# Kernel optimization log

Measured on AMD Instinct MI355X. Metric: run time of the kernel, lower is better.

## Reference

```python
import jax, jax.numpy as jnp
import numpy as np
import math

B, K, M, D = 8192, 16, 16, 256
LAMBDA_FGW = 0.5
TAU_KL = 0.1
N_OUTER = 5
N_SINKHORN = 10


def setup_inputs() -> dict:
    key = jax.random.key(0)
    ks = jax.random.split(key, 8)
    return {
        'slots_q': jax.random.normal(ks[0], (B, K, D), jnp.float32),
        'slots_r': jax.random.normal(ks[1], (B, M, D), jnp.float32),
        'mask_q': jnp.ones((B, K), jnp.float32),
        'mask_r': jnp.ones((B, M), jnp.float32),
        'centroids_q': jax.random.uniform(ks[2], (B, K, 2), jnp.float32),
        'centroids_r': jax.random.uniform(ks[3], (B, M, 2), jnp.float32),
        'W1': jax.random.normal(ks[4], (D, D), jnp.float32) * 0.05,
        'b1': jnp.zeros((D,), jnp.float32),
        'W2': jax.random.normal(ks[5], (D, D), jnp.float32) * 0.05,
        'b2': jnp.zeros((D,), jnp.float32),
        'log_eps': jnp.asarray(math.log(0.05), jnp.float32),
    }


def _pdist(a, b):
    # ||a_i - b_j||, clamped like torch: clamp(sumsq, 1e-6).sqrt()
    d2 = (jnp.sum(a * a, -1)[:, :, None] + jnp.sum(b * b, -1)[:, None, :]
          - 2.0 * jnp.einsum('bkd,bmd->bkm', a, b))
    return jnp.sqrt(jnp.clip(d2, 1e-6, None))


def reference(slots_q, slots_r, mask_q, mask_r, centroids_q, centroids_r,
              W1, b1, W2, b2, log_eps):
    proj = lambda x: jax.nn.relu(x @ W1.T + b1) @ W2.T + b2
    pq, pr = proj(slots_q), proj(slots_r)
    C = _pdist(pq, pr)                      # [B,K,M]
    Sq = _pdist(centroids_q, centroids_q)   # [B,K,K]
    Sr = _pdist(centroids_r, centroids_r)   # [B,M,M]

    mu = mask_q / (jnp.sum(mask_q, -1, keepdims=True) + 1e-8)
    nu = mask_r / (jnp.sum(mask_r, -1, keepdims=True) + 1e-8)
    T = mu[:, :, None] * nu[:, None, :]

    eps = jnp.clip(jnp.exp(log_eps), 0.01, 0.5)
    rho = TAU_KL / (TAU_KL + eps)
    log_mu = jnp.log(jnp.clip(mu, 1e-8, None))
    log_nu = jnpp = jnp.log(jnp.clip(nu, 1e-8, None))
    Sq2, Sr2 = Sq * Sq, Sr * Sr

    C_fgw = C
    for _ in range(N_OUTER):
        t1 = jnp.einsum('bkl,bl->bk', Sq2, T.sum(2))[:, :, None]
        t2 = jnp.einsum('bm,bmn->bn', T.sum(1), Sr2)[:, None, :]
        t3 = -2.0 * jnp.einsum('bkl,blm,bmn->bkn', Sq, T, Sr)
        L_gw = t1 + t2 + t3
        C_fgw = (1.0 - LAMBDA_FGW) * C + LAMBDA_FGW * L_gw
        log_K = -C_fgw / eps
        log_u = jnp.zeros_like(mu)
        log_v = jnp.zeros_like(nu)
        for _ in range(N_SINKHORN):
            log_u = rho * (log_mu - jax.nn.logsumexp(log_K + log_v[:, None, :], axis=2))
            log_v = rho * (log_nu - jax.nn.logsumexp(log_K + log_u[:, :, None], axis=1))
        T = jnp.exp(log_u[:, :, None] + log_K + log_v[:, None, :])

    cost = jnp.sum(T * C_fgw, axis=(-1, -2))
    return (jax.nn.sigmoid(-cost), T, C, cost)
```

## Files before the change

### kernel.cpp

```cpp
#include <hip/hip_runtime.h>


#define OFF_T   8192
#define OFF_C   2105344
#define OFF_CST 4202496

typedef float  f32x4  __attribute__((ext_vector_type(4)));
typedef float  f32x16 __attribute__((ext_vector_type(16)));
typedef short  s16x8  __attribute__((ext_vector_type(8)));

#define LOG2E 1.4426950408889634f

__device__ __forceinline__ float fexp2(float x) { return __builtin_amdgcn_exp2f(x); }
__device__ __forceinline__ float flog2(float x) { return __builtin_amdgcn_logf(x); }

__device__ __forceinline__ unsigned int cvt_pk_bf16(float lo, float hi) {
  unsigned int r;
  asm("v_cvt_pk_bf16_f32 %0, %1, %2" : "=v"(r) : "v"(lo), "v"(hi));
  return r;
}
__device__ __forceinline__ unsigned short cvt_bf16(float x) {
  unsigned int r;
  asm("v_cvt_pk_bf16_f32 %0, %1, %2" : "=v"(r) : "v"(x), "v"(x));
  return (unsigned short)r;
}

template <int CTRL>
__device__ __forceinline__ float dpp_add(float x) {
  return x + __int_as_float(__builtin_amdgcn_update_dpp(
      0, __float_as_int(x), CTRL, 0xf, 0xf, true));
}
template <int CTRL>
__device__ __forceinline__ float dpp_max(float x) {
  return fmaxf(x, __int_as_float(__builtin_amdgcn_update_dpp(
      0, __float_as_int(x), CTRL, 0xf, 0xf, true)));
}
__device__ __forceinline__ float row16_sum(float x) {
  x = dpp_add<0xB1>(x);  x = dpp_add<0x4E>(x);
  x = dpp_add<0x124>(x); x = dpp_add<0x128>(x);
  return x;
}
__device__ __forceinline__ float row16_max(float x) {
  x = dpp_max<0xB1>(x);  x = dpp_max<0x4E>(x);
  x = dpp_max<0x124>(x); x = dpp_max<0x128>(x);
  return x;
}
__device__ __forceinline__ float xor16_add(float x) {
  return x + __int_as_float(__builtin_amdgcn_ds_swizzle(__float_as_int(x), 0x401F));
}
__device__ __forceinline__ float xor16_max(float x) {
  return fmaxf(x, __int_as_float(__builtin_amdgcn_ds_swizzle(__float_as_int(x), 0x401F)));
}
__device__ __forceinline__ float xor32_add(float x) { return x + __shfl_xor(x, 32); }
__device__ __forceinline__ float xor32_max(float x) { return fmaxf(x, __shfl_xor(x, 32)); }

__global__ __launch_bounds__(256, 1)
void prep_w32(const float* __restrict__ W1, const float* __restrict__ W2,
              unsigned int* __restrict__ wh)
{
  const int fid  = blockIdx.x * 256 + threadIdx.x;
  const int l    = fid >> 13;
  const int s    = (fid >> 9) & 15;
  const int cg   = (fid >> 6) & 7;
  const int lane = fid & 63;
  const int col  = cg * 32 + (lane & 31);
  const int k0   = s * 16 + ((lane >> 5) << 3);
  const float* W = l ? W2 : W1;
  const float* src = W + ((size_t)col << 8) + k0;
  float4 a = *(const float4*)src;
  float4 b = *(const float4*)(src + 4);
  uint4 vh = {cvt_pk_bf16(a.x, a.y), cvt_pk_bf16(a.z, a.w),
              cvt_pk_bf16(b.x, b.y), cvt_pk_bf16(b.z, b.w)};
  ((uint4*)wh)[fid] = vh;
}

__global__ __launch_bounds__(512, 2)
void fgw_proj(const float* __restrict__ g_q,  const float* __restrict__ g_r,
              const unsigned short* __restrict__ wh,
              const float* __restrict__ g_b1, const float* __restrict__ g_b2,
              float* __restrict__ g_out)
{
  __shared__ __align__(16) float smemf[8704];
  char* sm = (char*)smemf;
  float* normL = smemf + 8192;
  const int bId0 = blockIdx.x * 2;
  const int tid  = threadIdx.x;
  const int lane = tid & 63, wid = tid >> 6;
  const int cl   = lane & 31, half = lane >> 5;

  #pragma unroll
  for (int j = 0; j < 4; ++j) {
    int idx = (j << 9) + tid;
    int bb  = idx >> 10;
    int t   = idx & 1023;
    int r   = t >> 6;
    int sg  = t & 63;
    int off = ((sg << 3) ^ ((r & 15) << 4));
    char* xb = sm + bb * 16384;
    const f32x4* xq = (const f32x4*)(g_q + (size_t)(bId0 + bb) * 4096 + (r << 8) + (sg << 2));
    const f32x4* xr = (const f32x4*)(g_r + (size_t)(bId0 + bb) * 4096 + (r << 8) + (sg << 2));
    f32x4 v0 = __builtin_nontemporal_load(xq);
    f32x4 v1 = __builtin_nontemporal_load(xr);
    {
      unsigned int* ph = (unsigned int*)(xb + r * 512 + off);
      ph[0] = cvt_pk_bf16(v0[0], v0[1]);
      ph[1] = cvt_pk_bf16(v0[2], v0[3]);
    }
    {
      unsigned int* ph = (unsigned int*)(xb + (16 + r) * 512 + off);
      ph[0] = cvt_pk_bf16(v1[0], v1[1]);
      ph[1] = cvt_pk_bf16(v1[2], v1[3]);
    }
  }
  __syncthreads();

  for (int layer = 0; layer < 2; ++layer) {
    f32x16 acc0, acc1;
    #pragma unroll
    for (int i = 0; i < 16; ++i) { acc0[i] = 0.f; acc1[i] = 0.f; }

    const float* bl_ = layer ? g_b2 : g_b1;
    const size_t base = (((size_t)layer * 16) * 8 + wid) * 64 + lane;

    s16x8 wfrag[16];
    #pragma unroll
    for (int ks = 0; ks < 16; ++ks)
      wfrag[ks] = *(const s16x8*)(wh + (base + (size_t)ks * 512) * 8);

    #pragma unroll
    for (int ks = 0; ks < 16; ++ks) {
      const int aoff = (((ks << 5) + (half << 4)) ^ ((cl & 15) << 4));
      s16x8 a0 = *(const s16x8*)(sm +         cl * 512 + aoff);
      s16x8 a1 = *(const s16x8*)(sm + 16384 + cl * 512 + aoff);
      acc0 = __builtin_amdgcn_mfma_f32_32x32x16_bf16(a0, wfrag[ks], acc0, 0, 0, 0);
      acc1 = __builtin_amdgcn_mfma_f32_32x32x16_bf16(a1, wfrag[ks], acc1, 0, 0, 0);
    }
    __syncthreads();

    const float bv  = bl_[(wid << 5) + cl];
    const int  colb = (((wid << 5) + cl) << 1);

    if (layer == 0) {
      #pragma unroll
      for (int reg = 0; reg < 16; ++reg) {
        int rr  = (reg & 3) + ((reg >> 2) << 3) + (half << 2);
        int off = colb ^ ((rr & 15) << 4);
        *(unsigned short*)(sm +         rr * 512 + off) = cvt_bf16(fmaxf(acc0[reg] + bv, 0.f));
        *(unsigned short*)(sm + 16384 + rr * 512 + off) = cvt_bf16(fmaxf(acc1[reg] + bv, 0.f));
      }
      __syncthreads();
    } else {
      #pragma unroll
      for (int reg = 0; reg < 16; ++reg) {
        int rr  = (reg & 3) + ((reg >> 2) << 3) + (half << 2);
        int off = colb ^ ((rr & 15) << 4);
        float p0 = acc0[reg] + bv, p1 = acc1[reg] + bv;
        float s0 = xor16_add(row16_sum(p0 * p0));
        float s1 = xor16_add(row16_sum(p1 * p1));
        if (cl == 0) {
          normL[(0 * 8 + wid) * 32 + rr] = s0;
          normL[(1 * 8 + wid) * 32 + rr] = s1;
        }
        *(unsigned short*)(sm +         rr * 512 + off) = cvt_bf16(p0);
        *(unsigned short*)(sm + 16384 + rr * 512 + off) = cvt_bf16(p1);
      }
      __syncthreads();
    }
  }

  if (wid >= 2) return;
  {
    const int fr = lane & 15, fg = lane >> 4;
    char* xg = sm + wid * 16384;
    f32x4 accG = {0.f, 0.f, 0.f, 0.f};
    #pragma unroll
    for (int ks16 = 0; ks16 < 8; ++ks16) {
      int koff = ((ks16 << 6) + (fg << 4)) ^ ((fr & 15) << 4);
      s16x8 aq = *(const s16x8*)(xg +        fr * 512 + koff);
      s16x8 br = *(const s16x8*)(xg + (16 + fr) * 512 + koff);
      accG = __builtin_amdgcn_mfma_f32_16x16x32_bf16(aq, br, accG, 0, 0, 0);
    }
    float nr_ = 0.f;
    #pragma unroll
    for (int cg = 0; cg < 8; ++cg) nr_ += normL[(wid * 8 + cg) * 32 + 16 + fr];
    #pragma unroll
    for (int j = 0; j < 4; ++j) {
      int row = (fg << 2) + j;
      float nq_ = 0.f;
      #pragma unroll
      for (int cg = 0; cg < 8; ++cg) nq_ += normL[(wid * 8 + cg) * 32 + row];
      float Cv = sqrtf(fmaxf(nq_ + nr_ - 2.0f * accG[j], 1e-6f));
      __builtin_nontemporal_store(Cv, g_out + OFF_C + (size_t)(bId0 + wid) * 256 + row * 16 + fr);
    }
  }
}

__global__ __launch_bounds__(256, 8)
void fgw_sink(const float* __restrict__ g_mq, const float* __restrict__ g_mr,
              const float* __restrict__ g_cq, const float* __restrict__ g_cr,
              const float* __restrict__ g_leps, float* __restrict__ g_out)
{
  __shared__ __align__(16) float sk[4 * 1088];
  const int tid  = threadIdx.x, lane = tid & 63, w = tid >> 6;
  const int batch = blockIdx.x * 4 + w;
  const int m = lane & 15, g = lane >> 4;
  float* L     = sk + w * 1088;
  float* SqL   = L;        float* SrL   = L + 320;
  float* TtL   = L + 640;  float* M1L   = L + 640;
  float* lmuL  = L + 960;  float* muL   = L + 976;
  float* cqxL  = L + 992;  float* cqyL  = L + 1008;
  float* crxL  = L + 1024; float* cryL  = L + 1040;
  float* trowL = L + 1056; float* tcolL = L + 1072;

  float mqv = g_mq[(size_t)batch * 16 + m];
  float mrv = g_mr[(size_t)batch * 16 + m];
  float mu_m = mqv / (row16_sum(mqv) + 1e-8f);
  float nu_m = mrv / (row16_sum(mrv) + 1e-8f);
  float lmu_m = __logf(fmaxf(mu_m, 1e-8f));
  float lnu_m = __logf(fmaxf(nu_m, 1e-8f));
  float cqx_m = g_cq[(size_t)batch * 32 + 2 * m];
  float cqy_m = g_cq[(size_t)batch * 32 + 2 * m + 1];
  float crx_m = g_cr[(size_t)batch * 32 + 2 * m];
  float cry_m = g_cr[(size_t)batch * 32 + 2 * m + 1];
  if (g == 0) {
    lmuL[m] = lmu_m;  muL[m] = mu_m;
    cqxL[m] = cqx_m;  cqyL[m] = cqy_m;
    crxL[m] = crx_m;  cryL[m] = cry_m;
  }
  f32x4 lmu_j = *(const f32x4*)(lmuL + 4 * g);
  f32x4 mu_j  = *(const f32x4*)(muL  + 4 * g);
  f32x4 cqxj  = *(const f32x4*)(cqxL + 4 * g);
  f32x4 cqyj  = *(const f32x4*)(cqyL + 4 * g);
  f32x4 crxj  = *(const f32x4*)(crxL + 4 * g);
  f32x4 cryj  = *(const f32x4*)(cryL + 4 * g);

  float Sq2r[4], Sr2r[4];
  #pragma unroll
  for (int j = 0; j < 4; ++j) {
    float dx = cqxj[j] - cqx_m, dy = cqyj[j] - cqy_m;
    float d2 = fmaxf(dx * dx + dy * dy, 1e-6f);
    SqL[(4 * g + j) * 20 + m] = sqrtf(d2);
    Sq2r[j] = d2;
    float ex = crxj[j] - crx_m, ey = cryj[j] - cry_m;
    float e2 = fmaxf(ex * ex + ey * ey, 1e-6f);
    SrL[(4 * g + j) * 20 + m] = sqrtf(e2);
    Sr2r[j] = e2;
  }

  float C_[4];
  const float* Cp = g_out + OFF_C + (size_t)batch * 256;
  #pragma unroll
  for (int j = 0; j < 4; ++j) C_[j] = Cp[(4 * g + j) * 16 + m];
  float eps = fminf(fmaxf(__expf(g_leps[0]), 0.01f), 0.5f);
  const float inv_eps = 1.0f / eps;
  const float rho = 0.1f / (0.1f + eps);
  const float k2s = -inv_eps * LOG2E;
  float rlmu2[4];
  #pragma unroll
  for (int j = 0; j < 4; ++j) rlmu2[j] = rho * lmu_j[j] * LOG2E;
  const float rlnu2 = rho * lnu_m * LOG2E;
  float T_[4];
  #pragma unroll
  for (int j = 0; j < 4; ++j) T_[j] = mu_j[j] * nu_m;

  float Cf[4], E[4], B2[4], x2[4], v2 = 0.f;

  for (int it = 0; it < 5; ++it) {
    float trow_j[4];
    #pragma unroll
    for (int j = 0; j < 4; ++j) trow_j[j] = row16_sum(T_[j]);
    float tc = xor32_add(xor16_add(T_[0] + T_[1] + T_[2] + T_[3]));
    if (m == 0) { f32x4 tv = {trow_j[0], trow_j[1], trow_j[2], trow_j[3]};
                  *(f32x4*)(trowL + 4 * g) = tv; }
    if (g == 0) tcolL[m] = tc;
    { f32x4 tv = {T_[0], T_[1], T_[2], T_[3]};
      *(f32x4*)(TtL + m * 20 + 4 * g) = tv; }

    float trow_m = trowL[m];
    float t1_[4];
    #pragma unroll
    for (int j = 0; j < 4; ++j) t1_[j] = row16_sum(Sq2r[j] * trow_m);
    f32x4 tcv = *(const f32x4*)(tcolL + 4 * g);
    float p2 = tcv[0] * Sr2r[0] + tcv[1] * Sr2r[1] + tcv[2] * Sr2r[2] + tcv[3] * Sr2r[3];
    float t2_ = xor32_add(xor16_add(p2));

    float M1r[4] = {0.f, 0.f, 0.f, 0.f};
    #pragma unroll
    for (int l = 0; l < 16; ++l) {
      f32x4 t4 = *(const f32x4*)(TtL + l * 20 + 4 * g);
      float srv = SrL[l * 20 + m];
      M1r[0] += t4[0] * srv; M1r[1] += t4[1] * srv;
      M1r[2] += t4[2] * srv; M1r[3] += t4[3] * srv;
    }
    #pragma unroll
    for (int j = 0; j < 4; ++j) M1L[(4 * g + j) * 20 + m] = M1r[j];
    float t3_[4] = {0.f, 0.f, 0.f, 0.f};
    #pragma unroll
    for (int l = 0; l < 16; ++l) {
      f32x4 sq4 = *(const f32x4*)(SqL + l * 20 + 4 * g);
      float m1v = M1L[l * 20 + m];
      t3_[0] += sq4[0] * m1v; t3_[1] += sq4[1] * m1v;
      t3_[2] += sq4[2] * m1v; t3_[3] += sq4[3] * m1v;
    }

    #pragma unroll
    for (int j = 0; j < 4; ++j) {
      float lgw = t1_[j] + t2_ - 2.0f * t3_[j];
      Cf[j] = 0.5f * C_[j] + 0.5f * lgw;
      float lk2 = k2s * Cf[j];
      float mx2 = row16_max(lk2);
      E[j]  = fexp2(lk2 - mx2);
      B2[j] = lk2 + rlmu2[j] - rho * mx2;
    }

    v2 = 0.f;
    #pragma unroll 1
    for (int s = 0; s < 10; ++s) {
      float ev = fexp2(v2);
      #pragma unroll
      for (int j = 0; j < 4; ++j) {
        float sj = row16_sum(E[j] * ev);
        x2[j] = B2[j] - rho * flog2(sj);
      }
      float mx = fmaxf(fmaxf(x2[0], x2[1]), fmaxf(x2[2], x2[3]));
      mx = xor32_max(xor16_max(mx));
      float ss = fexp2(x2[0] - mx) + fexp2(x2[1] - mx)
               + fexp2(x2[2] - mx) + fexp2(x2[3] - mx);
      ss = xor32_add(xor16_add(ss));
      v2 = rlnu2 - rho * (mx + flog2(ss));
    }
    #pragma unroll
    for (int j = 0; j < 4; ++j) T_[j] = fexp2(x2[j] + v2);
  }

  float cp = T_[0] * Cf[0] + T_[1] * Cf[1] + T_[2] * Cf[2] + T_[3] * Cf[3];
  cp = xor32_add(xor16_add(row16_sum(cp)));
  float* To = g_out + OFF_T + (size_t)batch * 256;
  #pragma unroll
  for (int j = 0; j < 4; ++j)
    __builtin_nontemporal_store(T_[j], To + (4 * g + j) * 16 + m);
  if (lane == 0) {
    g_out[batch] = 1.0f / (1.0f + __expf(cp));
    g_out[OFF_CST + batch] = cp;
  }
}

extern "C" void kernel_launch(void* const* d_in, const int* in_sizes, int n_in,
                              void* d_out, int out_size, void* d_ws, size_t ws_size,
                              hipStream_t stream) {
  (void)in_sizes; (void)n_in; (void)out_size; (void)ws_size;
  unsigned int*   wh32 = (unsigned int*)d_ws;
  unsigned short* wh   = (unsigned short*)wh32;

  prep_w32<<<dim3(64), dim3(256), 0, stream>>>(
      (const float*)d_in[6], (const float*)d_in[8], wh32);
  fgw_proj<<<dim3(4096), dim3(512), 0, stream>>>(
      (const float*)d_in[0], (const float*)d_in[1], wh,
      (const float*)d_in[7], (const float*)d_in[9], (float*)d_out);
  fgw_sink<<<dim3(2048), dim3(256), 0, stream>>>(
      (const float*)d_in[2], (const float*)d_in[3],
      (const float*)d_in[4], (const float*)d_in[5],
      (const float*)d_in[10], (float*)d_out);
}
```

Baseline: 192.8 us.

## Halve proj block to 4 waves with 2 column groups each; hoist Sinkhorn max

The projection kernel now runs 256 threads per block, and each wave computes two 32-column groups with four accumulators. Weight fragments are loaded inside the k-loop instead of being preloaded into 16 registers, and the launch bounds and shared memory size change to match. In the Sinkhorn loop, the per-iteration log-sum-exp max over x2 is replaced by a max over B2 computed once. Because x2 = B2 - rho*log(sum) with a positive sum, this shifted max is valid only while exp2 stays in range. The intent is better MFMA operand reuse, more blocks per CU, and fewer cross-lane reductions, at some risk of numeric underflow or overflow.

```diff
diff --git a/kernel.cpp b/kernel.cpp
--- a/kernel.cpp
+++ b/kernel.cpp
@@ -74,23 +74,24 @@
   ((uint4*)wh)[fid] = vh;
 }
 
-__global__ __launch_bounds__(512, 2)
+__global__ __launch_bounds__(256, 3)
 void fgw_proj(const float* __restrict__ g_q,  const float* __restrict__ g_r,
               const unsigned short* __restrict__ wh,
               const float* __restrict__ g_b1, const float* __restrict__ g_b2,
               float* __restrict__ g_out)
 {
-  __shared__ __align__(16) float smemf[8704];
+  __shared__ __align__(16) float smemf[8448];
   char* sm = (char*)smemf;
   float* normL = smemf + 8192;
   const int bId0 = blockIdx.x * 2;
   const int tid  = threadIdx.x;
   const int lane = tid & 63, wid = tid >> 6;
   const int cl   = lane & 31, half = lane >> 5;
-
-  #pragma unroll
-  for (int j = 0; j < 4; ++j) {
-    int idx = (j << 9) + tid;
+  const int cg0  = (wid << 1), cg1 = (wid << 1) + 1;
+
+  #pragma unroll
+  for (int j = 0; j < 8; ++j) {
+    int idx = (j << 8) + tid;
     int bb  = idx >> 10;
     int t   = idx & 1023;
     int r   = t >> 6;
@@ -115,54 +116,61 @@
   __syncthreads();
 
   for (int layer = 0; layer < 2; ++layer) {
-    f32x16 acc0, acc1;
-    #pragma unroll
-    for (int i = 0; i < 16; ++i) { acc0[i] = 0.f; acc1[i] = 0.f; }
+    f32x16 acc00, acc01, acc10, acc11;
+    #pragma unroll
+    for (int i = 0; i < 16; ++i) { acc00[i]=0.f; acc01[i]=0.f; acc10[i]=0.f; acc11[i]=0.f; }
 
     const float* bl_ = layer ? g_b2 : g_b1;
-    const size_t base = (((size_t)layer * 16) * 8 + wid) * 64 + lane;
-
-    s16x8 wfrag[16];
-    #pragma unroll
-    for (int ks = 0; ks < 16; ++ks)
-      wfrag[ks] = *(const s16x8*)(wh + (base + (size_t)ks * 512) * 8);
-
     #pragma unroll
     for (int ks = 0; ks < 16; ++ks) {
+      const size_t f0 = ((((size_t)layer * 16 + ks) * 8 + cg0) * 64 + lane) * 8;
+      s16x8 w0 = *(const s16x8*)(wh + f0);
+      s16x8 w1 = *(const s16x8*)(wh + f0 + 512);
       const int aoff = (((ks << 5) + (half << 4)) ^ ((cl & 15) << 4));
       s16x8 a0 = *(const s16x8*)(sm +         cl * 512 + aoff);
       s16x8 a1 = *(const s16x8*)(sm + 16384 + cl * 512 + aoff);
-      acc0 = __builtin_amdgcn_mfma_f32_32x32x16_bf16(a0, wfrag[ks], acc0, 0, 0, 0);
-      acc1 = __builtin_amdgcn_mfma_f32_32x32x16_bf16(a1, wfrag[ks], acc1, 0, 0, 0);
+      acc00 = __builtin_amdgcn_mfma_f32_32x32x16_bf16(a0, w0, acc00, 0, 0, 0);
+      acc01 = __builtin_amdgcn_mfma_f32_32x32x16_bf16(a0, w1, acc01, 0, 0, 0);
+      acc10 = __builtin_amdgcn_mfma_f32_32x32x16_bf16(a1, w0, acc10, 0, 0, 0);
+      acc11 = __builtin_amdgcn_mfma_f32_32x32x16_bf16(a1, w1, acc11, 0, 0, 0);
     }
     __syncthreads();
 
-    const float bv  = bl_[(wid << 5) + cl];
-    const int  colb = (((wid << 5) + cl) << 1);
+    const float bv0  = bl_[(cg0 << 5) + cl];
+    const float bv1  = bl_[(cg1 << 5) + cl];
+    const int colb0  = (((cg0 << 5) + cl) << 1);
+    const int colb1  = (((cg1 << 5) + cl) << 1);
 
     if (layer == 0) {
       #pragma unroll
       for (int reg = 0; reg < 16; ++reg) {
-        int rr  = (reg & 3) + ((reg >> 2) << 3) + (half << 2);
-        int off = colb ^ ((rr & 15) << 4);
-        *(unsigned short*)(sm +         rr * 512 + off) = cvt_bf16(fmaxf(acc0[reg] + bv, 0.f));
-        *(unsigned short*)(sm + 16384 + rr * 512 + off) = cvt_bf16(fmaxf(acc1[reg] + bv, 0.f));
+        int rr   = (reg & 3) + ((reg >> 2) << 3) + (half << 2);
+        int off0 = colb0 ^ ((rr & 15) << 4);
+        int off1 = colb1 ^ ((rr & 15) << 4);
+        *(unsigned short*)(sm +         rr * 512 + off0) = cvt_bf16(fmaxf(acc00[reg] + bv0, 0.f));
+        *(unsigned short*)(sm +         rr * 512 + off1) = cvt_bf16(fmaxf(acc01[reg] + bv1, 0.f));
+        *(unsigned short*)(sm + 16384 + rr * 512 + off0) = cvt_bf16(fmaxf(acc10[reg] + bv0, 0.f));
+        *(unsigned short*)(sm + 16384 + rr * 512 + off1) = cvt_bf16(fmaxf(acc11[reg] + bv1, 0.f));
       }
       __syncthreads();
     } else {
       #pragma unroll
       for (int reg = 0; reg < 16; ++reg) {
-        int rr  = (reg & 3) + ((reg >> 2) << 3) + (half << 2);
-        int off = colb ^ ((rr & 15) << 4);
-        float p0 = acc0[reg] + bv, p1 = acc1[reg] + bv;
-        float s0 = xor16_add(row16_sum(p0 * p0));
-        float s1 = xor16_add(row16_sum(p1 * p1));
+        int rr   = (reg & 3) + ((reg >> 2) << 3) + (half << 2);
+        int off0 = colb0 ^ ((rr & 15) << 4);
+        int off1 = colb1 ^ ((rr & 15) << 4);
+        float p00 = acc00[reg] + bv0, p01 = acc01[reg] + bv1;
+        float p10 = acc10[reg] + bv0, p11 = acc11[reg] + bv1;
+        float s0 = xor16_add(row16_sum(p00 * p00 + p01 * p01));
+        float s1 = xor16_add(row16_sum(p10 * p10 + p11 * p11));
         if (cl == 0) {
-          normL[(0 * 8 + wid) * 32 + rr] = s0;
-          normL[(1 * 8 + wid) * 32 + rr] = s1;
+          normL[(0 * 4 + wid) * 32 + rr] = s0;
+          normL[(1 * 4 + wid) * 32 + rr] = s1;
         }
-        *(unsigned short*)(sm +         rr * 512 + off) = cvt_bf16(p0);
-        *(unsigned short*)(sm + 16384 + rr * 512 + off) = cvt_bf16(p1);
+        *(unsigned short*)(sm +         rr * 512 + off0) = cvt_bf16(p00);
+        *(unsigned short*)(sm +         rr * 512 + off1) = cvt_bf16(p01);
+        *(unsigned short*)(sm + 16384 + rr * 512 + off0) = cvt_bf16(p10);
+        *(unsigned short*)(sm + 16384 + rr * 512 + off1) = cvt_bf16(p11);
       }
       __syncthreads();
     }
@@ -182,13 +190,13 @@
     }
     float nr_ = 0.f;
     #pragma unroll
-    for (int cg = 0; cg < 8; ++cg) nr_ += normL[(wid * 8 + cg) * 32 + 16 + fr];
+    for (int cg = 0; cg < 4; ++cg) nr_ += normL[(wid * 4 + cg) * 32 + 16 + fr];
     #pragma unroll
     for (int j = 0; j < 4; ++j) {
       int row = (fg << 2) + j;
       float nq_ = 0.f;
       #pragma unroll
-      for (int cg = 0; cg < 8; ++cg) nq_ += normL[(wid * 8 + cg) * 32 + row];
+      for (int cg = 0; cg < 4; ++cg) nq_ += normL[(wid * 4 + cg) * 32 + row];
       float Cv = sqrtf(fmaxf(nq_ + nr_ - 2.0f * accG[j], 1e-6f));
       __builtin_nontemporal_store(Cv, g_out + OFF_C + (size_t)(bId0 + wid) * 256 + row * 16 + fr);
     }
@@ -312,6 +320,8 @@
       E[j]  = fexp2(lk2 - mx2);
       B2[j] = lk2 + rlmu2[j] - rho * mx2;
     }
+    float mxB = fmaxf(fmaxf(B2[0], B2[1]), fmaxf(B2[2], B2[3]));
+    mxB = xor32_max(xor16_max(mxB));
 
     v2 = 0.f;
     #pragma unroll 1
@@ -322,12 +332,10 @@
         float sj = row16_sum(E[j] * ev);
         x2[j] = B2[j] - rho * flog2(sj);
       }
-      float mx = fmaxf(fmaxf(x2[0], x2[1]), fmaxf(x2[2], x2[3]));
-      mx = xor32_max(xor16_max(mx));
-      float ss = fexp2(x2[0] - mx) + fexp2(x2[1] - mx)
-               + fexp2(x2[2] - mx) + fexp2(x2[3] - mx);
+      float ss = fexp2(x2[0] - mxB) + fexp2(x2[1] - mxB)
+               + fexp2(x2[2] - mxB) + fexp2(x2[3] - mxB);
       ss = xor32_add(xor16_add(ss));
-      v2 = rlnu2 - rho * (mx + flog2(ss));
+      v2 = rlnu2 - rho * (mxB + flog2(ss));
     }
     #pragma unroll
     for (int j = 0; j < 4; ++j) T_[j] = fexp2(x2[j] + v2);
@@ -354,7 +362,7 @@
 
   prep_w32<<<dim3(64), dim3(256), 0, stream>>>(
       (const float*)d_in[6], (const float*)d_in[8], wh32);
-  fgw_proj<<<dim3(4096), dim3(512), 0, stream>>>(
+  fgw_proj<<<dim3(4096), dim3(256), 0, stream>>>(
       (const float*)d_in[0], (const float*)d_in[1], wh,
       (const float*)d_in[7], (const float*)d_in[9], (float*)d_out);
   fgw_sink<<<dim3(2048), dim3(256), 0, stream>>>(
```

Measured after the change: 191.4 us. About the same (-0.7%).
